# Optimization experiments

Hardware: AMD Instinct MI355X
Metric: run time of the kernel (lower is better)

The kernel has to match this reference:

```python
import jax, jax.numpy as jnp
import numpy as np


def setup_inputs() -> dict:
    key = jax.random.key(0)
    k1, k2 = jax.random.split(key)
    x = jax.random.normal(k1, (32, 256, 56, 56), dtype=jnp.float32)
    # Conv2d(2 -> 1, kernel 7x7, bias=False): weight [out_c=1, in_c=2, 7, 7]
    w_conv = jax.random.normal(k2, (1, 2, 7, 7), dtype=jnp.float32) * 0.1
    return {"x": x, "w_conv": w_conv}


def reference(x, w_conv):
    # channel-wise average and max pooling -> [B, 2, H, W]
    avgout = jnp.mean(x, axis=1, keepdims=True)
    maxout = jnp.max(x, axis=1, keepdims=True)
    x1 = jnp.concatenate([avgout, maxout], axis=1)
    # 7x7 conv, padding=3 (SAME), NCHW / OIHW
    x1 = jax.lax.conv_general_dilated(
        x1, w_conv,
        window_strides=(1, 1),
        padding=((3, 3), (3, 3)),
        dimension_numbers=("NCHW", "OIHW", "NCHW"),
    )
    gate = jax.nn.sigmoid(x1)  # [B, 1, H, W]
    return x * gate
```

## Files before the change

kernel.cpp:

```cpp
#include <hip/hip_runtime.h>
#include <hip/hip_bf16.h>
#include <math.h>

#define B_  32
#define C_  256
#define H_  56
#define W_  56
#define HW_ (H_ * W_)
#define BHW_ (B_ * HW_)

__global__ __launch_bounds__(256) void sa_reduce_kernel(
    const float* __restrict__ x, float* __restrict__ pool) {
  const int tx = threadIdx.x & 63;
  const int ty = threadIdx.x >> 6;
  const long base_pos = (long)blockIdx.x * 64;
  const int b = (int)(base_pos / HW_);
  const int hw0 = (int)(base_pos % HW_);
  const float* xp = x + (long)b * C_ * HW_ + hw0 + tx;

  float s = 0.f;
  float m = -INFINITY;
#pragma unroll 8
  for (int c = ty; c < C_; c += 4) {
    float v = xp[(long)c * HW_];
    s += v;
    m = fmaxf(m, v);
  }

  __shared__ float ssum[4][64];
  __shared__ float smax[4][64];
  ssum[ty][tx] = s;
  smax[ty][tx] = m;
  __syncthreads();

  if (ty == 0) {
    float S = ssum[0][tx] + ssum[1][tx] + ssum[2][tx] + ssum[3][tx];
    float M = fmaxf(fmaxf(smax[0][tx], smax[1][tx]),
                    fmaxf(smax[2][tx], smax[3][tx]));
    float* pb = pool + (long)b * 2 * HW_ + hw0 + tx;
    pb[0]   = S * (1.0f / (float)C_);
    pb[HW_] = M;
  }
}

__global__ __launch_bounds__(256) void sa_conv_kernel(
    const float* __restrict__ pool, const float* __restrict__ wt,
    float* __restrict__ gate) {
  int idx = blockIdx.x * blockDim.x + threadIdx.x;
  if (idx >= BHW_) return;
  const int b = idx / HW_;
  const int hw = idx % HW_;
  const int h = hw / W_;
  const int w = hw % W_;

  const float* p = pool + (long)b * 2 * HW_;
  float acc = 0.f;
#pragma unroll
  for (int ic = 0; ic < 2; ++ic) {
#pragma unroll
    for (int kh = 0; kh < 7; ++kh) {
      const int ih = h + kh - 3;
      if (ih < 0 || ih >= H_) continue;
      const float* row = p + ic * HW_ + ih * W_;
      const float* wr = wt + (ic * 7 + kh) * 7;
#pragma unroll
      for (int kw = 0; kw < 7; ++kw) {
        const int iw = w + kw - 3;
        if (iw < 0 || iw >= W_) continue;
        acc = fmaf(row[iw], wr[kw], acc);
      }
    }
  }
  gate[idx] = 1.0f / (1.0f + __expf(-acc));
}

#define HW4_ (HW_ / 4)
__global__ __launch_bounds__(256) void sa_mul_kernel(
    const float* __restrict__ x, const float* __restrict__ gate,
    float* __restrict__ out) {
  const long total4 = (long)B_ * C_ * HW4_;
  long i = (long)blockIdx.x * blockDim.x + threadIdx.x;
  if (i >= total4) return;
  const int hw4 = (int)(i % HW4_);
  const long bc = i / HW4_;
  const int b = (int)(bc / C_);

  float4 xv = ((const float4*)x)[i];
  float4 gv = ((const float4*)gate)[(long)b * HW4_ + hw4];
  float4 ov;
  ov.x = xv.x * gv.x;
  ov.y = xv.y * gv.y;
  ov.z = xv.z * gv.z;
  ov.w = xv.w * gv.w;
  ((float4*)out)[i] = ov;
}

extern "C" void kernel_launch(void* const* d_in, const int* in_sizes, int n_in,
                              void* d_out, int out_size, void* d_ws, size_t ws_size,
                              hipStream_t stream) {
  const float* x  = (const float*)d_in[0];
  const float* wc = (const float*)d_in[1];
  float* out = (float*)d_out;

  float* pool = (float*)d_ws;
  float* gate = pool + (long)B_ * 2 * HW_;

  sa_reduce_kernel<<<BHW_ / 64, 256, 0, stream>>>(x, pool);

  sa_conv_kernel<<<(BHW_ + 255) / 256, 256, 0, stream>>>(pool, wc, gate);

  const long total4 = (long)B_ * C_ * HW4_;
  sa_mul_kernel<<<(int)((total4 + 255) / 256), 256, 0, stream>>>(x, gate, out);
}
```

Measured before the change: 210.0 us.

## Fuse conv+sigmoid into gating multiply and vectorize channel reduction

The channel reduction now uses float4 loads, with 8 channel groups of 32 lanes per block. The 7x7 conv and sigmoid are folded into the multiply kernel: each block computes gates for its 128 positions, split across two threads per position by input channel, stores them in shared memory, then scales all 256 channels with nontemporal stores. This removes one launch and the gate buffer round trip. The cost is that each block redundantly reads pool neighbourhoods, and the conv work now delays the streaming loop inside the same block.

```diff
diff --git a/kernel.cpp b/kernel.cpp
--- a/kernel.cpp
+++ b/kernel.cpp
@@ -1,68 +1,90 @@
 #include <hip/hip_runtime.h>
-#include <hip/hip_bf16.h>
 #include <math.h>
 
-#define B_  32
-#define C_  256
-#define H_  56
-#define W_  56
-#define HW_ (H_ * W_)
-#define BHW_ (B_ * HW_)
+#define B_    32
+#define C_    256
+#define H_    56
+#define W_    56
+#define HW_   (H_ * W_)
+#define BHW_  (B_ * HW_)
+#define HW4_  (HW_ / 4)
+#define NF4_  (BHW_ / 4)
+#define CHUNKF4_ 32
+#define NBLK_ (NF4_ / CHUNKF4_)
+
+typedef float f4v __attribute__((ext_vector_type(4)));
 
 __global__ __launch_bounds__(256) void sa_reduce_kernel(
     const float* __restrict__ x, float* __restrict__ pool) {
-  const int tx = threadIdx.x & 63;
-  const int ty = threadIdx.x >> 6;
-  const long base_pos = (long)blockIdx.x * 64;
-  const int b = (int)(base_pos / HW_);
-  const int hw0 = (int)(base_pos % HW_);
-  const float* xp = x + (long)b * C_ * HW_ + hw0 + tx;
+  const int t = threadIdx.x;
+  const int lane = t & 31;
+  const int cgrp = t >> 5;
+  const unsigned if4 = (unsigned)blockIdx.x * CHUNKF4_ + lane;
+  const unsigned b = if4 / HW4_;
+  const unsigned hw4 = if4 % HW4_;
 
-  float s = 0.f;
-  float m = -INFINITY;
+  const f4v* x4 = (const f4v*)x;
+  const unsigned base = (b * C_ + cgrp) * HW4_ + hw4;
+
+  f4v s = {0.f, 0.f, 0.f, 0.f};
+  f4v m = {-INFINITY, -INFINITY, -INFINITY, -INFINITY};
 #pragma unroll 8
-  for (int c = ty; c < C_; c += 4) {
-    float v = xp[(long)c * HW_];
+  for (int k = 0; k < 32; ++k) {
+    f4v v = x4[base + (unsigned)(k * 8) * HW4_];
     s += v;
-    m = fmaxf(m, v);
+    m = (f4v){fmaxf(m.x, v.x), fmaxf(m.y, v.y), fmaxf(m.z, v.z), fmaxf(m.w, v.w)};
   }
 
-  __shared__ float ssum[4][64];
-  __shared__ float smax[4][64];
-  ssum[ty][tx] = s;
-  smax[ty][tx] = m;
+  __shared__ f4v ssum[8][32];
+  __shared__ f4v smax[8][32];
+  ssum[cgrp][lane] = s;
+  smax[cgrp][lane] = m;
   __syncthreads();
 
-  if (ty == 0) {
-    float S = ssum[0][tx] + ssum[1][tx] + ssum[2][tx] + ssum[3][tx];
-    float M = fmaxf(fmaxf(smax[0][tx], smax[1][tx]),
-                    fmaxf(smax[2][tx], smax[3][tx]));
-    float* pb = pool + (long)b * 2 * HW_ + hw0 + tx;
-    pb[0]   = S * (1.0f / (float)C_);
-    pb[HW_] = M;
+  if (t < 32) {
+    f4v S = ssum[0][t];
+    f4v M = smax[0][t];
+#pragma unroll
+    for (int g = 1; g < 8; ++g) {
+      f4v sg = ssum[g][t];
+      f4v mg = smax[g][t];
+      S += sg;
+      M = (f4v){fmaxf(M.x, mg.x), fmaxf(M.y, mg.y), fmaxf(M.z, mg.z), fmaxf(M.w, mg.w)};
+    }
+    f4v* p4 = (f4v*)pool;
+    const unsigned jf4 = (unsigned)blockIdx.x * CHUNKF4_ + t;
+    const unsigned bb = jf4 / HW4_;
+    const unsigned hh = jf4 % HW4_;
+    p4[bb * 2 * HW4_ + hh]        = S * (1.0f / (float)C_);
+    p4[bb * 2 * HW4_ + HW4_ + hh] = M;
   }
 }
 
-__global__ __launch_bounds__(256) void sa_conv_kernel(
-    const float* __restrict__ pool, const float* __restrict__ wt,
-    float* __restrict__ gate) {
-  int idx = blockIdx.x * blockDim.x + threadIdx.x;
-  if (idx >= BHW_) return;
-  const int b = idx / HW_;
-  const int hw = idx % HW_;
-  const int h = hw / W_;
-  const int w = hw % W_;
+__global__ __launch_bounds__(256) void sa_conv_apply_kernel(
+    const float* __restrict__ x, const float* __restrict__ pool,
+    const float* __restrict__ wt, float* __restrict__ out) {
+  const int t = threadIdx.x;
 
-  const float* p = pool + (long)b * 2 * HW_;
-  float acc = 0.f;
-#pragma unroll
-  for (int ic = 0; ic < 2; ++ic) {
+  __shared__ float partial[256];
+  __shared__ f4v sgate4[CHUNKF4_];
+
+  {
+    const int pos = t >> 1;
+    const int ic = t & 1;
+    const unsigned p = (unsigned)blockIdx.x * 128 + (unsigned)pos;
+    const unsigned b = p / HW_;
+    const unsigned hw = p % HW_;
+    const int h = (int)(hw / W_);
+    const int w = (int)(hw % W_);
+    const float* pl = pool + ((long)b * 2 + ic) * HW_;
+    const float* wr0 = wt + ic * 49;
+    float acc = 0.f;
 #pragma unroll
     for (int kh = 0; kh < 7; ++kh) {
       const int ih = h + kh - 3;
       if (ih < 0 || ih >= H_) continue;
-      const float* row = p + ic * HW_ + ih * W_;
-      const float* wr = wt + (ic * 7 + kh) * 7;
+      const float* row = pl + ih * W_;
+      const float* wr = wr0 + kh * 7;
 #pragma unroll
       for (int kw = 0; kw < 7; ++kw) {
         const int iw = w + kw - 3;
@@ -70,29 +92,32 @@
         acc = fmaf(row[iw], wr[kw], acc);
       }
     }
+    partial[t] = acc;
   }
-  gate[idx] = 1.0f / (1.0f + __expf(-acc));
-}
+  __syncthreads();
+  if (t < 128) {
+    float a = partial[2 * t] + partial[2 * t + 1];
+    ((float*)sgate4)[t] = 1.0f / (1.0f + __expf(-a));
+  }
+  __syncthreads();
 
-#define HW4_ (HW_ / 4)
-__global__ __launch_bounds__(256) void sa_mul_kernel(
-    const float* __restrict__ x, const float* __restrict__ gate,
-    float* __restrict__ out) {
-  const long total4 = (long)B_ * C_ * HW4_;
-  long i = (long)blockIdx.x * blockDim.x + threadIdx.x;
-  if (i >= total4) return;
-  const int hw4 = (int)(i % HW4_);
-  const long bc = i / HW4_;
-  const int b = (int)(bc / C_);
-
-  float4 xv = ((const float4*)x)[i];
-  float4 gv = ((const float4*)gate)[(long)b * HW4_ + hw4];
-  float4 ov;
-  ov.x = xv.x * gv.x;
-  ov.y = xv.y * gv.y;
-  ov.z = xv.z * gv.z;
-  ov.w = xv.w * gv.w;
-  ((float4*)out)[i] = ov;
+  {
+    const int lane = t & 31;
+    const int cgrp = t >> 5;
+    const unsigned if4 = (unsigned)blockIdx.x * CHUNKF4_ + lane;
+    const unsigned b = if4 / HW4_;
+    const unsigned hw4 = if4 % HW4_;
+    const unsigned base = (b * C_ + cgrp) * HW4_ + hw4;
+    const f4v* x4 = (const f4v*)x;
+    f4v* o4 = (f4v*)out;
+    const f4v g = sgate4[lane];
+#pragma unroll 8
+    for (int k = 0; k < 32; ++k) {
+      const unsigned idx = base + (unsigned)(k * 8) * HW4_;
+      f4v v = x4[idx];
+      __builtin_nontemporal_store(v * g, &o4[idx]);
+    }
+  }
 }
 
 extern "C" void kernel_launch(void* const* d_in, const int* in_sizes, int n_in,
@@ -101,14 +126,8 @@
   const float* x  = (const float*)d_in[0];
   const float* wc = (const float*)d_in[1];
   float* out = (float*)d_out;
+  float* pool = (float*)d_ws;
 
-  float* pool = (float*)d_ws;
-  float* gate = pool + (long)B_ * 2 * HW_;
-
-  sa_reduce_kernel<<<BHW_ / 64, 256, 0, stream>>>(x, pool);
-
-  sa_conv_kernel<<<(BHW_ + 255) / 256, 256, 0, stream>>>(pool, wc, gate);
-
-  const long total4 = (long)B_ * C_ * HW4_;
-  sa_mul_kernel<<<(int)((total4 + 255) / 256), 256, 0, stream>>>(x, gate, out);
+  sa_reduce_kernel<<<NBLK_, 256, 0, stream>>>(x, pool);
+  sa_conv_apply_kernel<<<NBLK_, 256, 0, stream>>>(x, pool, wc, out);
 }
```

Measured after the change: 206.4 us. About the same (-1.7%).
